# Optimization experiments

Measured on AMD Instinct MI355X. Metric: run time of the kernel, lower is better.

Reference implementation:

```python
import jax, jax.numpy as jnp
import numpy as np

EPS = 1e-6
K = 20
NUM_OBJECTS = 50
OBJ_FEAT = 256
C_DIM = 128
HIDDEN = 128


def vn_linear(x, W):
    # x: [B, C, 3, ...]; W: [O, C] -> [B, O, 3, ...]
    return jnp.einsum('oc,bc...->bo...', W, x)


def vn_leaky(x, Wdir, slope):
    d = vn_linear(x, Wdir)
    dot = jnp.sum(x * d, axis=2, keepdims=True)
    dsq = jnp.sum(d * d, axis=2, keepdims=True)
    x_neg = x - (dot / (dsq + EPS)) * d
    return slope * x + (1.0 - slope) * jnp.where(dot >= 0, x, x_neg)


def vn_linear_leaky(x, Wfeat, Wdir, slope):
    pf = vn_linear(x, Wfeat)
    d = vn_linear(x, Wdir)
    dot = jnp.sum(pf * d, axis=2, keepdims=True)
    dsq = jnp.sum(d * d, axis=2, keepdims=True)
    p_neg = pf - (dot / (dsq + EPS)) * d
    return slope * pf + (1.0 - slope) * jnp.where(dot >= 0, pf, p_neg)


def resblock(x, fc0, fc1, a0, a1, sc):
    net = vn_linear(vn_leaky(x, a0, 0.0), fc0)
    dx = vn_linear(vn_leaky(net, a1, 0.0), fc1)
    return vn_linear(x, sc) + dx


def get_graph_feature_cross(x, k):
    # x: [B, 3, N] -> edge features [B, 3, 3, N, k]
    inner = -2.0 * jnp.einsum('bdn,bdm->bnm', x, x)
    xx = jnp.sum(x * x, axis=1)                       # [B, N]
    neg_dist = -xx[:, :, None] - inner - xx[:, None, :]  # [B, N, N]
    idx = jax.lax.top_k(neg_dist, k)[1]               # [B, N, k] nearest neighbors
    xt = jnp.transpose(x, (0, 2, 1))                  # [B, N, 3]
    nbr = jax.vmap(lambda pts, ind: pts[ind])(xt, idx)  # [B, N, k, 3]
    ctr = jnp.broadcast_to(xt[:, :, None, :], nbr.shape)
    cross = jnp.cross(nbr, ctr)
    feat = jnp.stack([nbr - ctr, ctr, cross], axis=3)  # [B, N, k, 3, 3]
    return jnp.transpose(feat, (0, 3, 4, 1, 2))


def mlp2(zf, w0, w1, w2):
    h = jax.nn.relu(zf @ w0.T)
    h = jax.nn.relu(h @ w1.T)
    return h @ w2.T


def setup_inputs():
    key = jax.random.key(0)
    ks = jax.random.split(key, 24)
    B, N = 4, 4096

    def rn(k, shape):
        return jax.random.normal(k, shape, dtype=jnp.float32) * (1.0 / np.sqrt(shape[-1]))

    return {
        'p': jax.random.normal(ks[0], (B, N, 3), dtype=jnp.float32),
        'z_idxs': jax.random.randint(ks[1], (B,), 0, NUM_OBJECTS),
        'z': jax.random.normal(ks[2], (NUM_OBJECTS, OBJ_FEAT), dtype=jnp.float32),
        'hw0': rn(ks[3], (OBJ_FEAT, OBJ_FEAT)),
        'hw1': rn(ks[4], (OBJ_FEAT, OBJ_FEAT)),
        'hw2': rn(ks[5], (C_DIM * HIDDEN, OBJ_FEAT)),
        'hb0': rn(ks[6], (OBJ_FEAT, OBJ_FEAT)),
        'hb1': rn(ks[7], (OBJ_FEAT, OBJ_FEAT)),
        'hb2': rn(ks[8], (C_DIM, OBJ_FEAT)),
        'conv_pos_feat': rn(ks[9], (128, 3)),
        'conv_pos_dir': rn(ks[10], (128, 3)),
        'fc_pos_w': rn(ks[11], (2 * HIDDEN, 128)),
        'blk_fc0': rn(ks[12], (5, HIDDEN, 2 * HIDDEN)),
        'blk_fc1': rn(ks[13], (5, HIDDEN, HIDDEN)),
        'blk_act0': rn(ks[14], (5, 2 * HIDDEN, 2 * HIDDEN)),
        'blk_act1': rn(ks[15], (5, HIDDEN, HIDDEN)),
        'blk_sc': rn(ks[16], (5, HIDDEN, 2 * HIDDEN)),
        'actc_dir': rn(ks[17], (HIDDEN, HIDDEN)),
    }


def reference(p, z_idxs, z, hw0, hw1, hw2, hb0, hb1, hb2, conv_pos_feat,
              conv_pos_dir, fc_pos_w, blk_fc0, blk_fc1, blk_act0, blk_act1,
              blk_sc, actc_dir):
    B = p.shape[0]
    x = jnp.transpose(p, (0, 2, 1))                       # [B, 3, N]
    feat = get_graph_feature_cross(x, K)                  # [B, 3, 3, N, k]
    net = vn_linear_leaky(feat, conv_pos_feat, conv_pos_dir, 0.2)  # [B,128,3,N,k]
    net = jnp.mean(net, axis=-1)                          # [B,128,3,N]
    net = vn_linear(net, fc_pos_w)                        # [B,256,3,N]
    for i in range(5):
        net = resblock(net, blk_fc0[i], blk_fc1[i], blk_act0[i], blk_act1[i], blk_sc[i])
        if i < 4:
            pooled = jnp.mean(net, axis=-1, keepdims=True)
            net = jnp.concatenate([net, jnp.broadcast_to(pooled, net.shape)], axis=1)
    net = vn_leaky(jnp.mean(net, axis=-1), actc_dir, 0.2)  # [B, HIDDEN, 3]
    zf = z[z_idxs]                                        # [B, OBJ_FEAT]
    w = mlp2(zf, hw0, hw1, hw2).reshape(B, C_DIM, HIDDEN)  # hypernet weights
    b = mlp2(zf, hb0, hb1, hb2)                           # [B, C_DIM]
    c = jnp.einsum('bhd,bch->bcd', net, w) + b[:, :, None]  # [B, C_DIM, 3]
    return c
```

## Files before the change

kernel.cpp:

```cpp
#include <hip/hip_runtime.h>
#include <hip/hip_fp16.h>
#include <cstdint>
#include <cstddef>

#define NPTS 4096
#define BATCH 4
#define KNN 20

typedef __half f16;
using f32x4 = __attribute__((ext_vector_type(4))) float;
using f16x8 = __attribute__((ext_vector_type(8))) _Float16;

__global__ __launch_bounds__(512) void knn_kernel(const float* __restrict__ p,
                                                  int* __restrict__ idx_out) {
    __shared__ float pts[12288];
    const int tid  = threadIdx.x;
    const int wave = tid >> 6, lane = tid & 63;
    const int b  = blockIdx.x >> 9;
    const int nb = ((blockIdx.x & 511) << 3) + wave;

    const float4* src4 = (const float4*)(p + (size_t)b * NPTS * 3);
    float4* dst4 = (float4*)pts;
    for (int i = tid; i < NPTS * 3 / 4; i += 512) dst4[i] = src4[i];
    __syncthreads();

    const float cx = pts[3 * nb], cy = pts[3 * nb + 1], cz = pts[3 * nb + 2];
    unsigned lst[4];
#pragma unroll
    for (int i = 0; i < 4; i++) lst[i] = 0xFFFFFFFFu;

    for (int t = 0; t < NPTS / 64; t++) {
        int m = (t << 6) + lane;
        float dx = pts[3 * m] - cx, dy = pts[3 * m + 1] - cy, dz = pts[3 * m + 2] - cz;
        float d = dx * dx + dy * dy + dz * dz;
        unsigned c = (__float_as_uint(d) & 0xFFFFF000u) | (unsigned)m;
#pragma unroll
        for (int j = 0; j < 4; j++) {
            unsigned lo = min(c, lst[j]);
            c = max(c, lst[j]);
            lst[j] = lo;
        }
    }

    unsigned lo = 0u, hi = 0xFFFFFFFFu;
    for (int it = 0; it < 32; it++) {
        unsigned mid = lo + ((hi - lo) >> 1);
        int cnt = __popcll(__ballot(lst[0] <= mid)) + __popcll(__ballot(lst[1] <= mid))
                + __popcll(__ballot(lst[2] <= mid)) + __popcll(__ballot(lst[3] <= mid));
        if (cnt >= KNN) hi = mid; else lo = mid + 1;
    }
    const unsigned T = hi;

    unsigned long long bl[4];
#pragma unroll
    for (int j = 0; j < 4; j++) bl[j] = __ballot(lst[j] <= T);
    const unsigned long long lmask = (lane == 63) ? ~0ull >> 1 : (1ull << lane) - 1;
    int base = 0;
    const size_t out_base = ((size_t)b * NPTS + nb) * KNN;
#pragma unroll
    for (int j = 0; j < 4; j++) {
        if (lst[j] <= T) {
            int pos = base + (int)__popcll(bl[j] & lmask);
            idx_out[out_base + pos] = (int)(lst[j] & 0xFFFu);
        }
        base += (int)__popcll(bl[j]);
    }
}

__global__ __launch_bounds__(128) void edgeconv_kernel(
    const float* __restrict__ p, const int* __restrict__ idx,
    const float* __restrict__ wf, const float* __restrict__ wd,
    f16* __restrict__ out) {
    __shared__ float e[KNN][6];
    const int col = blockIdx.x;
    const int b = col >> 12;
    const int tid = threadIdx.x;
    const float cx = p[(size_t)col * 3], cy = p[(size_t)col * 3 + 1], cz = p[(size_t)col * 3 + 2];
    if (tid < KNN) {
        int j = idx[(size_t)col * KNN + tid];
        const float* q = &p[((size_t)b * NPTS + j) * 3];
        float nx = q[0], ny = q[1], nz = q[2];
        e[tid][0] = nx - cx; e[tid][1] = ny - cy; e[tid][2] = nz - cz;
        e[tid][3] = ny * cz - nz * cy;
        e[tid][4] = nz * cx - nx * cz;
        e[tid][5] = nx * cy - ny * cx;
    }
    __syncthreads();
    const int o = tid;
    const float f0 = wf[o * 3], f1 = wf[o * 3 + 1], f2 = wf[o * 3 + 2];
    const float g0 = wd[o * 3], g1 = wd[o * 3 + 1], g2 = wd[o * 3 + 2];
    const float pc0 = f1 * cx, pc1 = f1 * cy, pc2 = f1 * cz;
    const float gc0 = g1 * cx, gc1 = g1 * cy, gc2 = g1 * cz;
    float a0 = 0.f, a1 = 0.f, a2 = 0.f;
    for (int k = 0; k < KNN; k++) {
        float d0 = e[k][0], d1 = e[k][1], d2 = e[k][2];
        float c0 = e[k][3], c1 = e[k][4], c2 = e[k][5];
        float pf0 = fmaf(f0, d0, fmaf(f2, c0, pc0));
        float pf1 = fmaf(f0, d1, fmaf(f2, c1, pc1));
        float pf2 = fmaf(f0, d2, fmaf(f2, c2, pc2));
        float dd0 = fmaf(g0, d0, fmaf(g2, c0, gc0));
        float dd1 = fmaf(g0, d1, fmaf(g2, c1, gc1));
        float dd2 = fmaf(g0, d2, fmaf(g2, c2, gc2));
        float dot = pf0 * dd0 + pf1 * dd1 + pf2 * dd2;
        float dsq = dd0 * dd0 + dd1 * dd1 + dd2 * dd2;
        float w = 0.8f * dot * __builtin_amdgcn_rcpf(dsq + 1e-6f);
        w = (dot >= 0.f) ? 0.f : w;
        a0 += pf0 - w * dd0;
        a1 += pf1 - w * dd1;
        a2 += pf2 - w * dd2;
    }
    const float inv = 1.f / (float)KNN;
    out[((size_t)col * 3 + 0) * 128 + o] = __float2half(a0 * inv);
    out[((size_t)col * 3 + 1) * 128 + o] = __float2half(a1 * inv);
    out[((size_t)col * 3 + 2) * 128 + o] = __float2half(a2 * inv);
}

template <int KIN>
__global__ __launch_bounds__(256) void resblock_kernel(
    const uint16_t* __restrict__ INg,
    const uint16_t* __restrict__ Wfcp,
    const uint16_t* __restrict__ Wa0,
    const uint16_t* __restrict__ Wfc0,
    const uint16_t* __restrict__ Wa1,
    const uint16_t* __restrict__ Wsc,
    const uint16_t* __restrict__ Wfc1,
    const float* __restrict__ PBg,
    const float* __restrict__ BAg,
    const float* __restrict__ BSCg,
    f16* __restrict__ OUTg,
    float* __restrict__ PPg) {
    constexpr int XRB  = (KIN == 256) ? 528 : 272;
    constexpr int INS_OFF = (KIN == 256) ? 13056 : 0;
    constexpr int H0_OFF  = (KIN == 256) ? 38400 : 14592;
    constexpr int MID_OFF = (KIN == 256) ? 0 : 27648;
    constexpr int LDS_SZ  = (KIN == 256) ? 51456 : 40704;
    __shared__ char lds[LDS_SZ];
    char* MBs = lds;
    char* INs = lds + INS_OFF;
    float* PBs = (float*)(lds + 13056);
    char* H0h = lds + H0_OFF;
    char* MID = lds + MID_OFF;

    const int tid = threadIdx.x;
    const int lane = tid & 63;
    const int wc = tid >> 6;
    const int gr0 = blockIdx.x * 48;
    const int b = blockIdx.x >> 8;

    if (KIN == 128) {
        for (int i = tid; i < 384; i += 256) PBs[i] = PBg[b * 384 + i];
    }
    {
        char* dst = (KIN == 256) ? MBs : INs;
#pragma unroll
        for (int j = 0; j < 3; j++) {
            int chunk = tid + j * 256;
            int row = chunk >> 4, c16 = chunk & 15;
            f16x8 v = *(const f16x8*)(INg + (size_t)(gr0 + row) * 128 + c16 * 8);
            *(f16x8*)(dst + row * 272 + c16 * 16) = v;
        }
    }
    __syncthreads();

    if (KIN == 256) {
        f32x4 acc[3][4];
#pragma unroll
        for (int i = 0; i < 3; i++)
#pragma unroll
            for (int j = 0; j < 4; j++) acc[i][j] = (f32x4){0.f, 0.f, 0.f, 0.f};
#pragma unroll
        for (int ks = 0; ks < 4; ks++) {
            const int kb = ks * 64 + (lane >> 4) * 16;
            f16x8 af[3], bf[4];
#pragma unroll
            for (int mi = 0; mi < 3; mi++) {
                int r = mi * 16 + (lane & 15);
                af[mi] = *(const f16x8*)(MBs + r * 272 + kb);
            }
#pragma unroll
            for (int ni = 0; ni < 4; ni++) {
                int o = wc * 64 + ni * 16 + (lane & 15);
                bf[ni] = *(const f16x8*)(Wfcp + o * 128 + ks * 32 + (lane >> 4) * 8);
            }
#pragma unroll
            for (int mi = 0; mi < 3; mi++)
#pragma unroll
                for (int ni = 0; ni < 4; ni++)
                    acc[mi][ni] = __builtin_amdgcn_mfma_f32_16x16x32_f16(
                        af[mi], bf[ni], acc[mi][ni], 0, 0, 0);
        }
#pragma unroll
        for (int mi = 0; mi < 3; mi++)
#pragma unroll
            for (int ni = 0; ni < 4; ni++) {
                int col = wc * 64 + ni * 16 + (lane & 15);
#pragma unroll
                for (int r = 0; r < 4; r++) {
                    int row = mi * 16 + (lane >> 4) * 4 + r;
                    *(f16*)(INs + row * XRB + col * 2) = __float2half(acc[mi][ni][r]);
                }
            }
        __syncthreads();
    }

    f32x4 midAcc[3][2];
#pragma unroll
    for (int i = 0; i < 3; i++) { midAcc[i][0] = (f32x4){0,0,0,0}; midAcc[i][1] = (f32x4){0,0,0,0}; }

#pragma unroll
    for (int half = 0; half < 2; half++) {
        {
            f32x4 acc[3][2];
#pragma unroll
            for (int i = 0; i < 3; i++) { acc[i][0] = (f32x4){0,0,0,0}; acc[i][1] = (f32x4){0,0,0,0}; }
#pragma unroll
            for (int ks = 0; ks < KIN / 32; ks++) {
                const int kb = ks * 64 + (lane >> 4) * 16;
                f16x8 af[3], bf[2];
#pragma unroll
                for (int mi = 0; mi < 3; mi++) {
                    int r = mi * 16 + (lane & 15);
                    af[mi] = *(const f16x8*)(INs + r * XRB + kb);
                }
#pragma unroll
                for (int ni = 0; ni < 2; ni++) {
                    int o = half * 128 + wc * 32 + ni * 16 + (lane & 15);
                    bf[ni] = *(const f16x8*)(Wa0 + o * 256 + ks * 32 + (lane >> 4) * 8);
                }
#pragma unroll
                for (int mi = 0; mi < 3; mi++)
#pragma unroll
                    for (int ni = 0; ni < 2; ni++)
                        acc[mi][ni] = __builtin_amdgcn_mfma_f32_16x16x32_f16(
                            af[mi], bf[ni], acc[mi][ni], 0, 0, 0);
            }
#pragma unroll
            for (int mi = 0; mi < 3; mi++)
#pragma unroll
                for (int ni = 0; ni < 2; ni++) {
                    int col = wc * 32 + ni * 16 + (lane & 15);
#pragma unroll
                    for (int r = 0; r < 4; r++) {
                        int row = mi * 16 + (lane >> 4) * 4 + r;
                        float v = acc[mi][ni][r];
                        if (KIN == 128)
                            v += BAg[b * 768 + (row % 3) * 256 + half * 128 + col];
                        *(f16*)(H0h + row * 272 + col * 2) = __float2half(v);
                    }
                }
        }
        __syncthreads();
#pragma unroll
        for (int j = 0; j < 4; j++) {
            int it = tid + j * 256;
            int pnt = it >> 6, cp = it & 63;
            float xv[3][2], dv[3][2];
#pragma unroll
            for (int s = 0; s < 3; s++) {
                int row = pnt * 3 + s;
                __half2 d2 = *(const __half2*)(H0h + row * 272 + cp * 4);
                dv[s][0] = __half2float(d2.x); dv[s][1] = __half2float(d2.y);
                if (KIN == 256) {
                    __half2 x2 = *(const __half2*)(INs + row * XRB + half * 256 + cp * 4);
                    xv[s][0] = __half2float(x2.x); xv[s][1] = __half2float(x2.y);
                } else {
                    if (half == 0) {
                        __half2 x2 = *(const __half2*)(INs + row * XRB + cp * 4);
                        xv[s][0] = __half2float(x2.x); xv[s][1] = __half2float(x2.y);
                    } else {
                        xv[s][0] = PBs[s * 128 + cp * 2];
                        xv[s][1] = PBs[s * 128 + cp * 2 + 1];
                    }
                }
            }
#pragma unroll
            for (int jj = 0; jj < 2; jj++) {
                float dot = xv[0][jj] * dv[0][jj] + xv[1][jj] * dv[1][jj] + xv[2][jj] * dv[2][jj];
                float dsq = dv[0][jj] * dv[0][jj] + dv[1][jj] * dv[1][jj] + dv[2][jj] * dv[2][jj];
                float coef = dot * __builtin_amdgcn_rcpf(dsq + 1e-6f);
                bool pos = dot >= 0.f;
#pragma unroll
                for (int s = 0; s < 3; s++)
                    xv[s][jj] = pos ? xv[s][jj] : xv[s][jj] - coef * dv[s][jj];
            }
#pragma unroll
            for (int s = 0; s < 3; s++) {
                int row = pnt * 3 + s;
                __half2 h2;
                h2.x = __float2half(xv[s][0]);
                h2.y = __float2half(xv[s][1]);
                *(__half2*)(H0h + row * 272 + cp * 4) = h2;
            }
        }
        __syncthreads();
#pragma unroll
        for (int ks = 0; ks < 4; ks++) {
            const int kb = ks * 64 + (lane >> 4) * 16;
            f16x8 af[3], bf[2];
#pragma unroll
            for (int mi = 0; mi < 3; mi++) {
                int r = mi * 16 + (lane & 15);
                af[mi] = *(const f16x8*)(H0h + r * 272 + kb);
            }
#pragma unroll
            for (int ni = 0; ni < 2; ni++) {
                int o = wc * 32 + ni * 16 + (lane & 15);
                bf[ni] = *(const f16x8*)(Wfc0 + o * 256 + half * 128 + ks * 32 + (lane >> 4) * 8);
            }
#pragma unroll
            for (int mi = 0; mi < 3; mi++)
#pragma unroll
                for (int ni = 0; ni < 2; ni++)
                    midAcc[mi][ni] = __builtin_amdgcn_mfma_f32_16x16x32_f16(
                        af[mi], bf[ni], midAcc[mi][ni], 0, 0, 0);
        }
        __syncthreads();
    }

#pragma unroll
    for (int mi = 0; mi < 3; mi++)
#pragma unroll
        for (int ni = 0; ni < 2; ni++) {
            int col = wc * 32 + ni * 16 + (lane & 15);
#pragma unroll
            for (int r = 0; r < 4; r++) {
                int row = mi * 16 + (lane >> 4) * 4 + r;
                *(f16*)(MID + row * 272 + col * 2) = __float2half(midAcc[mi][ni][r]);
            }
        }
    __syncthreads();

    {
        f32x4 acc[3][2];
#pragma unroll
        for (int i = 0; i < 3; i++) { acc[i][0] = (f32x4){0,0,0,0}; acc[i][1] = (f32x4){0,0,0,0}; }
#pragma unroll
        for (int ks = 0; ks < 4; ks++) {
            const int kb = ks * 64 + (lane >> 4) * 16;
            f16x8 af[3], bf[2];
#pragma unroll
            for (int mi = 0; mi < 3; mi++) {
                int r = mi * 16 + (lane & 15);
                af[mi] = *(const f16x8*)(MID + r * 272 + kb);
            }
#pragma unroll
            for (int ni = 0; ni < 2; ni++) {
                int o = wc * 32 + ni * 16 + (lane & 15);
                bf[ni] = *(const f16x8*)(Wa1 + o * 128 + ks * 32 + (lane >> 4) * 8);
            }
#pragma unroll
            for (int mi = 0; mi < 3; mi++)
#pragma unroll
                for (int ni = 0; ni < 2; ni++)
                    acc[mi][ni] = __builtin_amdgcn_mfma_f32_16x16x32_f16(
                        af[mi], bf[ni], acc[mi][ni], 0, 0, 0);
        }
#pragma unroll
        for (int mi = 0; mi < 3; mi++)
#pragma unroll
            for (int ni = 0; ni < 2; ni++) {
                int col = wc * 32 + ni * 16 + (lane & 15);
#pragma unroll
                for (int r = 0; r < 4; r++) {
                    int row = mi * 16 + (lane >> 4) * 4 + r;
                    *(f16*)(H0h + row * 272 + col * 2) = __float2half(acc[mi][ni][r]);
                }
            }
    }
    __syncthreads();
#pragma unroll
    for (int j = 0; j < 4; j++) {
        int it = tid + j * 256;
        int pnt = it >> 6, cp = it & 63;
        float xv[3][2], dv[3][2];
#pragma unroll
        for (int s = 0; s < 3; s++) {
            int row = pnt * 3 + s;
            __half2 d2 = *(const __half2*)(H0h + row * 272 + cp * 4);
            __half2 x2 = *(const __half2*)(MID + row * 272 + cp * 4);
            dv[s][0] = __half2float(d2.x); dv[s][1] = __half2float(d2.y);
            xv[s][0] = __half2float(x2.x); xv[s][1] = __half2float(x2.y);
        }
#pragma unroll
        for (int jj = 0; jj < 2; jj++) {
            float dot = xv[0][jj] * dv[0][jj] + xv[1][jj] * dv[1][jj] + xv[2][jj] * dv[2][jj];
            float dsq = dv[0][jj] * dv[0][jj] + dv[1][jj] * dv[1][jj] + dv[2][jj] * dv[2][jj];
            float coef = dot * __builtin_amdgcn_rcpf(dsq + 1e-6f);
            bool pos = dot >= 0.f;
#pragma unroll
            for (int s = 0; s < 3; s++)
                xv[s][jj] = pos ? xv[s][jj] : xv[s][jj] - coef * dv[s][jj];
        }
#pragma unroll
        for (int s = 0; s < 3; s++) {
            int row = pnt * 3 + s;
            __half2 h2;
            h2.x = __float2half(xv[s][0]);
            h2.y = __float2half(xv[s][1]);
            *(__half2*)(H0h + row * 272 + cp * 4) = h2;
        }
    }
    __syncthreads();

    {
        f32x4 acc[3][2];
#pragma unroll
        for (int i = 0; i < 3; i++) { acc[i][0] = (f32x4){0,0,0,0}; acc[i][1] = (f32x4){0,0,0,0}; }
        constexpr int NKS = (KIN + 128) / 32;
#pragma unroll
        for (int ks = 0; ks < NKS; ks++) {
            const int kelem = ks * 32;
            f16x8 af[3], bf[2];
            if (kelem < KIN) {
                const int kb = kelem * 2 + (lane >> 4) * 16;
#pragma unroll
                for (int mi = 0; mi < 3; mi++) {
                    int r = mi * 16 + (lane & 15);
                    af[mi] = *(const f16x8*)(INs + r * XRB + kb);
                }
#pragma unroll
                for (int ni = 0; ni < 2; ni++) {
                    int o = wc * 32 + ni * 16 + (lane & 15);
                    bf[ni] = *(const f16x8*)(Wsc + o * 256 + kelem + (lane >> 4) * 8);
                }
            } else {
                const int kk = kelem - KIN;
                const int kb = kk * 2 + (lane >> 4) * 16;
#pragma unroll
                for (int mi = 0; mi < 3; mi++) {
                    int r = mi * 16 + (lane & 15);
                    af[mi] = *(const f16x8*)(H0h + r * 272 + kb);
                }
#pragma unroll
                for (int ni = 0; ni < 2; ni++) {
                    int o = wc * 32 + ni * 16 + (lane & 15);
                    bf[ni] = *(const f16x8*)(Wfc1 + o * 128 + kk + (lane >> 4) * 8);
                }
            }
#pragma unroll
            for (int mi = 0; mi < 3; mi++)
#pragma unroll
                for (int ni = 0; ni < 2; ni++)
                    acc[mi][ni] = __builtin_amdgcn_mfma_f32_16x16x32_f16(
                        af[mi], bf[ni], acc[mi][ni], 0, 0, 0);
        }
        float ps[2][3] = {};
#pragma unroll
        for (int mi = 0; mi < 3; mi++)
#pragma unroll
            for (int ni = 0; ni < 2; ni++) {
                int col = wc * 32 + ni * 16 + (lane & 15);
#pragma unroll
                for (int r = 0; r < 4; r++) {
                    int row = mi * 16 + (lane >> 4) * 4 + r;
                    float v = acc[mi][ni][r];
                    if (KIN == 128) v += BSCg[b * 384 + (row % 3) * 128 + col];
                    OUTg[(size_t)(gr0 + row) * 128 + col] = __float2half(v);
                    ps[ni][row % 3] += v;
                }
            }
#pragma unroll
        for (int ni = 0; ni < 2; ni++)
#pragma unroll
            for (int s = 0; s < 3; s++) {
                float x = ps[ni][s];
                x += __shfl_xor(x, 16, 64);
                x += __shfl_xor(x, 32, 64);
                ps[ni][s] = x;
            }
        if ((lane >> 4) == 0) {
#pragma unroll
            for (int ni = 0; ni < 2; ni++) {
                int col = wc * 32 + ni * 16 + (lane & 15);
#pragma unroll
                for (int s = 0; s < 3; s++)
                    PPg[(size_t)blockIdx.x * 384 + s * 128 + col] = ps[ni][s];
            }
        }
    }
}

__global__ __launch_bounds__(512) void poolbias_kernel(
    const float* __restrict__ PP, const f16* __restrict__ a0n, const f16* __restrict__ scn,
    float* __restrict__ PB, float* __restrict__ BA, float* __restrict__ BSC, int hasbias) {
    __shared__ float red[4][128];
    __shared__ float pl[128];
    const int bs = blockIdx.x;
    const int b = bs / 3, s = bs % 3;
    const int t = threadIdx.x;
    const int col = t & 127, seg = t >> 7;
    {
        float acc = 0.f;
        const float* base = PP + (size_t)(b * 256) * 384 + s * 128 + col;
        for (int k = seg * 64; k < seg * 64 + 64; k++) acc += base[(size_t)k * 384];
        red[seg][col] = acc;
    }
    __syncthreads();
    if (t < 128) {
        float a = (red[0][t] + red[1][t]) + (red[2][t] + red[3][t]);
        a *= (1.f / (float)NPTS);
        pl[t] = a;
        PB[bs * 128 + t] = a;
    }
    __syncthreads();
    if (!hasbias) return;
    if (t < 256) {
        float s2 = 0.f;
        for (int c = 0; c < 128; c++) s2 += __half2float(a0n[t * 256 + 128 + c]) * pl[c];
        BA[bs * 256 + t] = s2;
    } else if (t < 384) {
        int o = t - 256;
        float s2 = 0.f;
        for (int c = 0; c < 128; c++) s2 += __half2float(scn[o * 256 + 128 + c]) * pl[c];
        BSC[bs * 128 + o] = s2;
    }
}

__global__ void cvt_all(const float* __restrict__ fcpw, const float* __restrict__ act0,
                        const float* __restrict__ fc0, const float* __restrict__ act1,
                        const float* __restrict__ fc1, const float* __restrict__ scw,
                        f16* o_fcpw, f16* o_act0, f16* o_fc0, f16* o_act1, f16* o_fc1,
                        f16* o_scw) {
    int i = blockIdx.x * 256 + threadIdx.x;
    if (i < 32768) { o_fcpw[i] = __float2half(fcpw[i]); }
    else if (i < 360448) { int j = i - 32768;  o_act0[j] = __float2half(act0[j]); }
    else if (i < 524288) { int j = i - 360448; o_fc0[j]  = __float2half(fc0[j]); }
    else if (i < 606208) { int j = i - 524288; o_act1[j] = __float2half(act1[j]); }
    else if (i < 688128) { int j = i - 606208; o_fc1[j]  = __float2half(fc1[j]); }
    else                 { int j = i - 688128; o_scw[j]  = __float2half(scw[j]); }
}

__global__ __launch_bounds__(256) void hypermlp_kernel(
    const float* __restrict__ z, const int* __restrict__ zidx,
    const float* __restrict__ hw0, const float* __restrict__ hw1,
    const float* __restrict__ hb0, const float* __restrict__ hb1,
    const float* __restrict__ hb2,
    float* __restrict__ H2, float* __restrict__ BV) {
    __shared__ float zf[256], ta[256], tb[256];
    const int b = blockIdx.x, o = threadIdx.x;
    zf[o] = z[(size_t)zidx[b] * 256 + o];
    __syncthreads();
    float s = 0.f;
    for (int c = 0; c < 256; c++) s += zf[c] * hw0[o * 256 + c];
    ta[o] = fmaxf(s, 0.f);
    __syncthreads();
    s = 0.f;
    for (int c = 0; c < 256; c++) s += ta[c] * hw1[o * 256 + c];
    tb[o] = fmaxf(s, 0.f);
    __syncthreads();
    H2[(size_t)b * 256 + o] = tb[o];
    s = 0.f;
    for (int c = 0; c < 256; c++) s += zf[c] * hb0[o * 256 + c];
    __syncthreads();
    ta[o] = fmaxf(s, 0.f);
    __syncthreads();
    s = 0.f;
    for (int c = 0; c < 256; c++) s += ta[c] * hb1[o * 256 + c];
    __syncthreads();
    tb[o] = fmaxf(s, 0.f);
    __syncthreads();
    if (o < 128) {
        s = 0.f;
        for (int c = 0; c < 256; c++) s += tb[c] * hb2[o * 256 + c];
        BV[(size_t)b * 128 + o] = s;
    }
}

__global__ __launch_bounds__(256) void wmat_kernel(const float* __restrict__ H2,
                                                   const float* __restrict__ hw2,
                                                   float* __restrict__ WM) {
    __shared__ float h[256];
    const int b = blockIdx.y;
    const int row = blockIdx.x * 256 + threadIdx.x;
    h[threadIdx.x] = H2[(size_t)b * 256 + threadIdx.x];
    __syncthreads();
    float s = 0.f;
    for (int c = 0; c < 256; c++) s += h[c] * hw2[(size_t)row * 256 + c];
    WM[(size_t)b * 16384 + row] = s;
}

__global__ __launch_bounds__(384) void final_out_kernel(
    const float* __restrict__ pb, const float* __restrict__ actc,
    const float* __restrict__ WM, const float* __restrict__ BV,
    float* __restrict__ out) {
    __shared__ float pb2s[3][128];
    const int b = blockIdx.x;
    const int t = threadIdx.x;
    if (t < 128) {
        const int o = t;
        float d0 = 0.f, d1 = 0.f, d2 = 0.f;
        for (int c = 0; c < 128; c++) {
            float w = actc[o * 128 + c];
            d0 += w * pb[(size_t)(b * 3 + 0) * 128 + c];
            d1 += w * pb[(size_t)(b * 3 + 1) * 128 + c];
            d2 += w * pb[(size_t)(b * 3 + 2) * 128 + c];
        }
        float x0 = pb[(size_t)(b * 3 + 0) * 128 + o];
        float x1 = pb[(size_t)(b * 3 + 1) * 128 + o];
        float x2 = pb[(size_t)(b * 3 + 2) * 128 + o];
        float dot = x0 * d0 + x1 * d1 + x2 * d2;
        float dsq = d0 * d0 + d1 * d1 + d2 * d2;
        float coef = dot / (dsq + 1e-6f);
        bool pos = dot >= 0.f;
        float h0 = pos ? x0 : x0 - coef * d0;
        float h1 = pos ? x1 : x1 - coef * d1;
        float h2 = pos ? x2 : x2 - coef * d2;
        pb2s[0][o] = 0.2f * x0 + 0.8f * h0;
        pb2s[1][o] = 0.2f * x1 + 0.8f * h1;
        pb2s[2][o] = 0.2f * x2 + 0.8f * h2;
    }
    __syncthreads();
    const int cd = t / 3, d = t % 3;
    float s = BV[(size_t)b * 128 + cd];
    for (int h = 0; h < 128; h++)
        s += pb2s[d][h] * WM[(size_t)b * 16384 + cd * 128 + h];
    out[(size_t)b * 384 + cd * 3 + d] = s;
}

extern "C" void kernel_launch(void* const* d_in, const int* in_sizes, int n_in,
                              void* d_out, int out_size, void* d_ws, size_t ws_size,
                              hipStream_t stream) {
    (void)in_sizes; (void)n_in; (void)out_size; (void)ws_size;
    const float* p     = (const float*)d_in[0];
    const int*   zidx  = (const int*)d_in[1];
    const float* z     = (const float*)d_in[2];
    const float* hw0   = (const float*)d_in[3];
    const float* hw1   = (const float*)d_in[4];
    const float* hw2   = (const float*)d_in[5];
    const float* hb0   = (const float*)d_in[6];
    const float* hb1   = (const float*)d_in[7];
    const float* hb2   = (const float*)d_in[8];
    const float* cpf   = (const float*)d_in[9];
    const float* cpd   = (const float*)d_in[10];
    const float* fcpw  = (const float*)d_in[11];
    const float* fc0w  = (const float*)d_in[12];
    const float* fc1w  = (const float*)d_in[13];
    const float* act0  = (const float*)d_in[14];
    const float* act1  = (const float*)d_in[15];
    const float* scw   = (const float*)d_in[16];
    const float* actc  = (const float*)d_in[17];
    float* out = (float*)d_out;
    char* ws = (char*)d_ws;

    int*   IDX   = (int*)(ws + 0);
    f16*   MB    = (f16*)(ws + 1310720);
    f16*   MB2   = (f16*)(ws + 13893632);
    f16*   FCPW16= (f16*)(ws + 26476544);
    f16*   ACT0W = (f16*)(ws + 26542080);
    f16*   FC0W  = (f16*)(ws + 27197440);
    f16*   ACT1W = (f16*)(ws + 27525120);
    f16*   FC1W  = (f16*)(ws + 27688960);
    f16*   SCW16 = (f16*)(ws + 27852800);
    float* PP    = (float*)(ws + 28180480);
    float* PB    = (float*)(ws + 29753344);
    float* H2    = (float*)(ws + 29759488);
    float* BV    = (float*)(ws + 29763584);
    float* WM    = (float*)(ws + 29765632);
    float* BA    = (float*)(ws + 30027776);
    float* BSC   = (float*)(ws + 30040064);

    cvt_all<<<3328, 256, 0, stream>>>(fcpw, act0, fc0w, act1, fc1w, scw,
                                      FCPW16, ACT0W, FC0W, ACT1W, FC1W, SCW16);

    knn_kernel<<<BATCH * NPTS / 8, 512, 0, stream>>>(p, IDX);
    edgeconv_kernel<<<BATCH * NPTS, 128, 0, stream>>>(p, IDX, cpf, cpd, MB);

    resblock_kernel<256><<<1024, 256, 0, stream>>>(
        (const uint16_t*)MB, (const uint16_t*)FCPW16,
        (const uint16_t*)ACT0W, (const uint16_t*)FC0W,
        (const uint16_t*)ACT1W, (const uint16_t*)SCW16, (const uint16_t*)FC1W,
        nullptr, nullptr, nullptr, MB2, PP);
    poolbias_kernel<<<12, 512, 0, stream>>>(PP, ACT0W + 1 * 65536, SCW16 + 1 * 32768,
                                            PB, BA, BSC, 1);

    for (int i = 1; i < 5; i++) {
        const f16* a0h = ACT0W + (size_t)i * 256 * 256;
        const f16* sch = SCW16 + (size_t)i * 128 * 256;
        f16* in  = (i & 1) ? MB2 : MB;
        f16* ob  = (i & 1) ? MB : MB2;
        resblock_kernel<128><<<1024, 256, 0, stream>>>(
            (const uint16_t*)in, nullptr,
            (const uint16_t*)a0h,
            (const uint16_t*)(FC0W + (size_t)i * 128 * 256),
            (const uint16_t*)(ACT1W + (size_t)i * 128 * 128),
            (const uint16_t*)sch,
            (const uint16_t*)(FC1W + (size_t)i * 128 * 128),
            PB, BA, BSC, ob, PP);
        if (i < 4) {
            poolbias_kernel<<<12, 512, 0, stream>>>(
                PP, ACT0W + (size_t)(i + 1) * 65536, SCW16 + (size_t)(i + 1) * 32768,
                PB, BA, BSC, 1);
        } else {
            poolbias_kernel<<<12, 512, 0, stream>>>(PP, nullptr, nullptr, PB, BA, BSC, 0);
        }
    }

    hypermlp_kernel<<<4, 256, 0, stream>>>(z, zidx, hw0, hw1, hb0, hb1, hb2, H2, BV);
    wmat_kernel<<<dim3(64, 4), 256, 0, stream>>>(H2, hw2, WM);
    final_out_kernel<<<4, 384, 0, stream>>>(PB, actc, WM, BV, out);
}
```

Measured before the change: 382.7 us.

## Fold fc_pos into first resblock's act0 and shortcut weights

Precomputes composed weight matrices act0·fc_pos and sc·fc_pos in a new small kernel, so the first resblock consumes the 128-channel edgeconv output directly for its direction and shortcut GEMMs. The full 256-channel fc_pos activation is now produced per half only for the leaky-ReLU x term, and the LDS footprint shrinks. This cuts the K dimension of the act0 and shortcut GEMMs from 256 to 128. It adds a naive fp32 compose kernel launch and a separate fp16 rounding of the composed weights.

```diff
diff --git a/kernel.cpp b/kernel.cpp
--- a/kernel.cpp
+++ b/kernel.cpp
@@ -115,6 +115,23 @@
     out[((size_t)col * 3 + 2) * 128 + o] = __float2half(a2 * inv);
 }
 
+__global__ __launch_bounds__(128) void compose_kernel(
+    const float* __restrict__ act0, const float* __restrict__ scw,
+    const float* __restrict__ fcpw, f16* __restrict__ A0F, f16* __restrict__ SCF) {
+    const int rowid = blockIdx.x;
+    const int c = threadIdx.x;
+    if (rowid < 256) {
+        float s = 0.f;
+        for (int k = 0; k < 256; k++) s += act0[rowid * 256 + k] * fcpw[k * 128 + c];
+        A0F[rowid * 128 + c] = __float2half(s);
+    } else {
+        const int o = rowid - 256;
+        float s = 0.f;
+        for (int k = 0; k < 256; k++) s += scw[o * 256 + k] * fcpw[k * 128 + c];
+        SCF[o * 128 + c] = __float2half(s);
+    }
+}
+
 template <int KIN>
 __global__ __launch_bounds__(256) void resblock_kernel(
     const uint16_t* __restrict__ INg,
@@ -129,15 +146,16 @@
     const float* __restrict__ BSCg,
     f16* __restrict__ OUTg,
     float* __restrict__ PPg) {
-    constexpr int XRB  = (KIN == 256) ? 528 : 272;
-    constexpr int INS_OFF = (KIN == 256) ? 13056 : 0;
-    constexpr int H0_OFF  = (KIN == 256) ? 38400 : 14592;
-    constexpr int MID_OFF = (KIN == 256) ? 0 : 27648;
-    constexpr int LDS_SZ  = (KIN == 256) ? 51456 : 40704;
+    constexpr int XRB = 272;
+    constexpr int XH_OFF  = (KIN == 256) ? 13056 : 0;
+    constexpr int PBS_OFF = 13056;
+    constexpr int H0_OFF  = (KIN == 256) ? 26112 : 14592;
+    constexpr int MID_OFF = (KIN == 256) ? 13056 : 27648;
+    constexpr int LDS_SZ  = (KIN == 256) ? 39168 : 40704;
     __shared__ char lds[LDS_SZ];
-    char* MBs = lds;
-    char* INs = lds + INS_OFF;
-    float* PBs = (float*)(lds + 13056);
+    char* INs = lds;
+    char* XH  = lds + XH_OFF;
+    float* PBs = (float*)(lds + PBS_OFF);
     char* H0h = lds + H0_OFF;
     char* MID = lds + MID_OFF;
 
@@ -151,57 +169,15 @@
         for (int i = tid; i < 384; i += 256) PBs[i] = PBg[b * 384 + i];
     }
     {
-        char* dst = (KIN == 256) ? MBs : INs;
 #pragma unroll
         for (int j = 0; j < 3; j++) {
             int chunk = tid + j * 256;
             int row = chunk >> 4, c16 = chunk & 15;
             f16x8 v = *(const f16x8*)(INg + (size_t)(gr0 + row) * 128 + c16 * 8);
-            *(f16x8*)(dst + row * 272 + c16 * 16) = v;
-        }
-    }
-    __syncthreads();
-
-    if (KIN == 256) {
-        f32x4 acc[3][4];
-#pragma unroll
-        for (int i = 0; i < 3; i++)
-#pragma unroll
-            for (int j = 0; j < 4; j++) acc[i][j] = (f32x4){0.f, 0.f, 0.f, 0.f};
-#pragma unroll
-        for (int ks = 0; ks < 4; ks++) {
-            const int kb = ks * 64 + (lane >> 4) * 16;
-            f16x8 af[3], bf[4];
-#pragma unroll
-            for (int mi = 0; mi < 3; mi++) {
-                int r = mi * 16 + (lane & 15);
-                af[mi] = *(const f16x8*)(MBs + r * 272 + kb);
-            }
-#pragma unroll
-            for (int ni = 0; ni < 4; ni++) {
-                int o = wc * 64 + ni * 16 + (lane & 15);
-                bf[ni] = *(const f16x8*)(Wfcp + o * 128 + ks * 32 + (lane >> 4) * 8);
-            }
-#pragma unroll
-            for (int mi = 0; mi < 3; mi++)
-#pragma unroll
-                for (int ni = 0; ni < 4; ni++)
-                    acc[mi][ni] = __builtin_amdgcn_mfma_f32_16x16x32_f16(
-                        af[mi], bf[ni], acc[mi][ni], 0, 0, 0);
-        }
-#pragma unroll
-        for (int mi = 0; mi < 3; mi++)
-#pragma unroll
-            for (int ni = 0; ni < 4; ni++) {
-                int col = wc * 64 + ni * 16 + (lane & 15);
-#pragma unroll
-                for (int r = 0; r < 4; r++) {
-                    int row = mi * 16 + (lane >> 4) * 4 + r;
-                    *(f16*)(INs + row * XRB + col * 2) = __float2half(acc[mi][ni][r]);
-                }
-            }
-        __syncthreads();
-    }
+            *(f16x8*)(INs + row * 272 + c16 * 16) = v;
+        }
+    }
+    __syncthreads();
 
     f32x4 midAcc[3][2];
 #pragma unroll
@@ -214,18 +190,21 @@
 #pragma unroll
             for (int i = 0; i < 3; i++) { acc[i][0] = (f32x4){0,0,0,0}; acc[i][1] = (f32x4){0,0,0,0}; }
 #pragma unroll
-            for (int ks = 0; ks < KIN / 32; ks++) {
+            for (int ks = 0; ks < 4; ks++) {
                 const int kb = ks * 64 + (lane >> 4) * 16;
                 f16x8 af[3], bf[2];
 #pragma unroll
                 for (int mi = 0; mi < 3; mi++) {
                     int r = mi * 16 + (lane & 15);
-                    af[mi] = *(const f16x8*)(INs + r * XRB + kb);
+                    af[mi] = *(const f16x8*)(INs + r * 272 + kb);
                 }
 #pragma unroll
                 for (int ni = 0; ni < 2; ni++) {
                     int o = half * 128 + wc * 32 + ni * 16 + (lane & 15);
-                    bf[ni] = *(const f16x8*)(Wa0 + o * 256 + ks * 32 + (lane >> 4) * 8);
+                    if (KIN == 256)
+                        bf[ni] = *(const f16x8*)(Wa0 + o * 128 + ks * 32 + (lane >> 4) * 8);
+                    else
+                        bf[ni] = *(const f16x8*)(Wa0 + o * 256 + ks * 32 + (lane >> 4) * 8);
                 }
 #pragma unroll
                 for (int mi = 0; mi < 3; mi++)
@@ -249,6 +228,43 @@
                     }
                 }
         }
+        if (KIN == 256) {
+            f32x4 acc[3][2];
+#pragma unroll
+            for (int i = 0; i < 3; i++) { acc[i][0] = (f32x4){0,0,0,0}; acc[i][1] = (f32x4){0,0,0,0}; }
+#pragma unroll
+            for (int ks = 0; ks < 4; ks++) {
+                const int kb = ks * 64 + (lane >> 4) * 16;
+                f16x8 af[3], bf[2];
+#pragma unroll
+                for (int mi = 0; mi < 3; mi++) {
+                    int r = mi * 16 + (lane & 15);
+                    af[mi] = *(const f16x8*)(INs + r * 272 + kb);
+                }
+#pragma unroll
+                for (int ni = 0; ni < 2; ni++) {
+                    int o = half * 128 + wc * 32 + ni * 16 + (lane & 15);
+                    bf[ni] = *(const f16x8*)(Wfcp + o * 128 + ks * 32 + (lane >> 4) * 8);
+                }
+#pragma unroll
+                for (int mi = 0; mi < 3; mi++)
+#pragma unroll
+                    for (int ni = 0; ni < 2; ni++)
+                        acc[mi][ni] = __builtin_amdgcn_mfma_f32_16x16x32_f16(
+                            af[mi], bf[ni], acc[mi][ni], 0, 0, 0);
+            }
+#pragma unroll
+            for (int mi = 0; mi < 3; mi++)
+#pragma unroll
+                for (int ni = 0; ni < 2; ni++) {
+                    int col = wc * 32 + ni * 16 + (lane & 15);
+#pragma unroll
+                    for (int r = 0; r < 4; r++) {
+                        int row = mi * 16 + (lane >> 4) * 4 + r;
+                        *(f16*)(XH + row * 272 + col * 2) = __float2half(acc[mi][ni][r]);
+                    }
+                }
+        }
         __syncthreads();
 #pragma unroll
         for (int j = 0; j < 4; j++) {
@@ -261,11 +277,11 @@
                 __half2 d2 = *(const __half2*)(H0h + row * 272 + cp * 4);
                 dv[s][0] = __half2float(d2.x); dv[s][1] = __half2float(d2.y);
                 if (KIN == 256) {
-                    __half2 x2 = *(const __half2*)(INs + row * XRB + half * 256 + cp * 4);
+                    __half2 x2 = *(const __half2*)(XH + row * 272 + cp * 4);
                     xv[s][0] = __half2float(x2.x); xv[s][1] = __half2float(x2.y);
                 } else {
                     if (half == 0) {
-                        __half2 x2 = *(const __half2*)(INs + row * XRB + cp * 4);
+                        __half2 x2 = *(const __half2*)(INs + row * 272 + cp * 4);
                         xv[s][0] = __half2float(x2.x); xv[s][1] = __half2float(x2.y);
                     } else {
                         xv[s][0] = PBs[s * 128 + cp * 2];
@@ -406,25 +422,27 @@
         f32x4 acc[3][2];
 #pragma unroll
         for (int i = 0; i < 3; i++) { acc[i][0] = (f32x4){0,0,0,0}; acc[i][1] = (f32x4){0,0,0,0}; }
-        constexpr int NKS = (KIN + 128) / 32;
-#pragma unroll
-        for (int ks = 0; ks < NKS; ks++) {
+#pragma unroll
+        for (int ks = 0; ks < 8; ks++) {
             const int kelem = ks * 32;
             f16x8 af[3], bf[2];
-            if (kelem < KIN) {
+            if (kelem < 128) {
                 const int kb = kelem * 2 + (lane >> 4) * 16;
 #pragma unroll
                 for (int mi = 0; mi < 3; mi++) {
                     int r = mi * 16 + (lane & 15);
-                    af[mi] = *(const f16x8*)(INs + r * XRB + kb);
+                    af[mi] = *(const f16x8*)(INs + r * 272 + kb);
                 }
 #pragma unroll
                 for (int ni = 0; ni < 2; ni++) {
                     int o = wc * 32 + ni * 16 + (lane & 15);
-                    bf[ni] = *(const f16x8*)(Wsc + o * 256 + kelem + (lane >> 4) * 8);
+                    if (KIN == 256)
+                        bf[ni] = *(const f16x8*)(Wsc + o * 128 + kelem + (lane >> 4) * 8);
+                    else
+                        bf[ni] = *(const f16x8*)(Wsc + o * 256 + kelem + (lane >> 4) * 8);
                 }
             } else {
-                const int kk = kelem - KIN;
+                const int kk = kelem - 128;
                 const int kb = kk * 2 + (lane >> 4) * 16;
 #pragma unroll
                 for (int mi = 0; mi < 3; mi++) {
@@ -658,17 +676,20 @@
     float* WM    = (float*)(ws + 29765632);
     float* BA    = (float*)(ws + 30027776);
     float* BSC   = (float*)(ws + 30040064);
+    f16*   A0F   = (f16*)(ws + 30046208);
+    f16*   SCF   = (f16*)(ws + 30111744);
 
     cvt_all<<<3328, 256, 0, stream>>>(fcpw, act0, fc0w, act1, fc1w, scw,
                                       FCPW16, ACT0W, FC0W, ACT1W, FC1W, SCW16);
+    compose_kernel<<<384, 128, 0, stream>>>(act0, scw, fcpw, A0F, SCF);
 
     knn_kernel<<<BATCH * NPTS / 8, 512, 0, stream>>>(p, IDX);
     edgeconv_kernel<<<BATCH * NPTS, 128, 0, stream>>>(p, IDX, cpf, cpd, MB);
 
     resblock_kernel<256><<<1024, 256, 0, stream>>>(
         (const uint16_t*)MB, (const uint16_t*)FCPW16,
-        (const uint16_t*)ACT0W, (const uint16_t*)FC0W,
-        (const uint16_t*)ACT1W, (const uint16_t*)SCW16, (const uint16_t*)FC1W,
+        (const uint16_t*)A0F, (const uint16_t*)FC0W,
+        (const uint16_t*)ACT1W, (const uint16_t*)SCF, (const uint16_t*)FC1W,
         nullptr, nullptr, nullptr, MB2, PP);
     poolbias_kernel<<<12, 512, 0, stream>>>(PP, ACT0W + 1 * 65536, SCW16 + 1 * 32768,
                                             PB, BA, BSC, 1);
```

Result: no change. 379.9 us (-0.7%).
